# Kernel optimization log

Measured on AMD Instinct MI355X. Metric: run time of the kernel, lower is better.

Reference implementation:

```python
import jax, jax.numpy as jnp
import numpy as np

N_NODES = 100000  # static segment count for segment_sum
DEGREE = 2        # polynomial degree of the Laplacian filter


def setup_inputs() -> dict:
    key = jax.random.key(0)
    k1, k2, k3, k4 = jax.random.split(key, 4)
    N, E, C = N_NODES, 1600000, 32
    x = jax.random.normal(k1, (N, C), dtype=jnp.float32)
    weights = jax.random.normal(k2, (1 + DEGREE,), dtype=jnp.float32)
    edge_src = jax.random.randint(k3, (E,), 0, N, dtype=jnp.int32)
    edge_dst = jax.random.randint(k4, (E,), 0, N, dtype=jnp.int32)
    return {"x": x, "weights": weights, "edge_src": edge_src, "edge_dst": edge_dst}


def reference(x, weights, edge_src, edge_dst):
    """y = (w0 * I + w1 * L + ... + w_d * L^d) @ x with L = D - A,
    computed by the recurrence t_k = L @ t_{k-1} (never materializing L^k)."""
    N = N_NODES
    # node degrees: D[i] = number of edges landing on i
    deg = jax.ops.segment_sum(jnp.ones_like(edge_src, dtype=x.dtype), edge_dst,
                              num_segments=N)  # [N]

    def lap_matvec(t):
        # (L @ t)[i] = deg[i] * t[i] - sum_{(s->i) in E} t[s]
        agg = jax.ops.segment_sum(t[edge_src], edge_dst, num_segments=N)  # [N, C]
        return deg[:, None] * t - agg

    y = weights[0] * x
    t = x
    for k in range(1, 1 + DEGREE):  # fixed small loop over polynomial order
        t = lap_matvec(t)
        y = y + weights[k] * t
    return y
```

## Files before the change

kernel.cpp:

```cpp
#include <hip/hip_runtime.h>

#define C 32
#define NT 256
#define BSH 8
#define BNODE 256
#define CAPC 5632
#define SRCMASK 0x1FFFF

__device__ __forceinline__ unsigned int f2bf(float f) {
    unsigned int u = __float_as_uint(f);
    return (u + 0x7FFFu + ((u >> 16) & 1u)) >> 16;
}
__device__ __forceinline__ float bflo(unsigned int u) { return __uint_as_float(u << 16); }
__device__ __forceinline__ float bfhi(unsigned int u) { return __uint_as_float(u & 0xFFFF0000u); }

__global__ void init_cursor(int* __restrict__ cursor, int nbuck) {
    int i = blockIdx.x * blockDim.x + threadIdx.x;
    if (i < nbuck) cursor[i] = i * CAPC;
}

__global__ void cvt_kernel(const float2* __restrict__ x2, unsigned int* __restrict__ xb, int n2) {
    int i = blockIdx.x * blockDim.x + threadIdx.x;
    if (i >= n2) return;
    float2 v = x2[i];
    xb[i] = f2bf(v.x) | (f2bf(v.y) << 16);
}

__global__ __launch_bounds__(1024) void phaseA(const int* __restrict__ src,
                                               const int* __restrict__ dst,
                                               int* __restrict__ cursor,
                                               int* __restrict__ pk,
                                               int E, int nbuck, int chunk) {
    extern __shared__ int l[];
    int* lcnt = l;
    int* lcur = l + nbuck;
    int tid = threadIdx.x;
    for (int i = tid; i < nbuck; i += 1024) lcnt[i] = 0;
    __syncthreads();
    int base = blockIdx.x * chunk;
    int end  = min(base + chunk, E);
    for (int e = base + tid; e < end; e += 1024)
        atomicAdd(&lcnt[dst[e] >> BSH], 1);
    __syncthreads();
    for (int i = tid; i < nbuck; i += 1024) {
        int c = lcnt[i];
        lcur[i] = c ? atomicAdd(&cursor[i], c) : 0;
    }
    __syncthreads();
    for (int e = base + tid; e < end; e += 1024) {
        int d = dst[e];
        int b = d >> BSH;
        int pos = atomicAdd(&lcur[b], 1);
        pk[pos] = src[e] | ((d & (BNODE - 1)) << 17);
    }
}

__global__ __launch_bounds__(512) void phaseB(int* __restrict__ pk,
                                              const int* __restrict__ cursor,
                                              int* __restrict__ row_start,
                                              int* __restrict__ ideg, int N) {
    __shared__ int ent[CAPC];
    __shared__ int h[BNODE];
    __shared__ int s[BNODE];
    __shared__ int cur[BNODE];
    int b = blockIdx.x;
    int tid = threadIdx.x;
    int base = b * CAPC;
    int cnt = min(cursor[b] - base, CAPC);
    for (int i = tid; i < cnt; i += 512) ent[i] = pk[base + i];
    if (tid < BNODE) h[tid] = 0;
    __syncthreads();
    for (int i = tid; i < cnt; i += 512) atomicAdd(&h[ent[i] >> 17], 1);
    __syncthreads();
    int v = 0;
    if (tid < BNODE) { v = h[tid]; s[tid] = v; }
    __syncthreads();
    for (int off = 1; off < BNODE; off <<= 1) {
        int u = 0;
        if (tid < BNODE && tid >= off) u = s[tid - off];
        __syncthreads();
        if (tid < BNODE) s[tid] += u;
        __syncthreads();
    }
    if (tid < BNODE) {
        int exc = s[tid] - v;
        int n = (b << BSH) + tid;
        if (n < N) { row_start[n] = base + exc; ideg[n] = v; }
        cur[tid] = exc;
    }
    __syncthreads();
    for (int i = tid; i < cnt; i += 512) {
        int en = ent[i];
        int pos = atomicAdd(&cur[en >> 17], 1);
        pk[base + pos] = en & SRCMASK;
    }
}

__global__ __launch_bounds__(NT) void gather1_bf(const float* __restrict__ x,
        const unsigned int* __restrict__ xb, const int* __restrict__ pk,
        const int* __restrict__ row_start, const int* __restrict__ ideg,
        float* __restrict__ t1, unsigned int* __restrict__ t1b, int N) {
    int g = blockIdx.x * blockDim.x + threadIdx.x;
    int n = g >> 4;
    if (n >= N) return;
    int l = g & 15;
    int rs = row_start[n];
    int dg = ideg[n];
    int re = rs + dg;
    float ax0=0,ay0=0,ax1=0,ay1=0,ax2=0,ay2=0,ax3=0,ay3=0;
    int j = rs;
    for (; j + 3 < re; j += 4) {
        int s0 = pk[j], s1 = pk[j+1], s2 = pk[j+2], s3 = pk[j+3];
        unsigned int u0 = xb[s0*16 + l], u1 = xb[s1*16 + l];
        unsigned int u2 = xb[s2*16 + l], u3 = xb[s3*16 + l];
        ax0 += bflo(u0); ay0 += bfhi(u0);
        ax1 += bflo(u1); ay1 += bfhi(u1);
        ax2 += bflo(u2); ay2 += bfhi(u2);
        ax3 += bflo(u3); ay3 += bfhi(u3);
    }
    for (; j < re; ++j) { unsigned int u = xb[pk[j]*16 + l]; ax0 += bflo(u); ay0 += bfhi(u); }
    float sx = (ax0+ax1)+(ax2+ax3), sy = (ay0+ay1)+(ay2+ay3);
    size_t o = (size_t)n * C + l * 2;
    float2 xv = *(const float2*)(x + o);
    float fdg = (float)dg;
    float2 tv; tv.x = fdg * xv.x - sx; tv.y = fdg * xv.y - sy;
    *(float2*)(t1 + o) = tv;
    t1b[n*16 + l] = f2bf(tv.x) | (f2bf(tv.y) << 16);
}

__global__ __launch_bounds__(NT) void gather2_bf(const float* __restrict__ x,
        const float* __restrict__ t1, const unsigned int* __restrict__ t1b,
        const int* __restrict__ pk, const int* __restrict__ row_start,
        const int* __restrict__ ideg, const float* __restrict__ wts,
        float* __restrict__ y, int N) {
    int g = blockIdx.x * blockDim.x + threadIdx.x;
    int n = g >> 4;
    if (n >= N) return;
    int l = g & 15;
    int rs = row_start[n];
    int dg = ideg[n];
    int re = rs + dg;
    float ax0=0,ay0=0,ax1=0,ay1=0,ax2=0,ay2=0,ax3=0,ay3=0;
    int j = rs;
    for (; j + 3 < re; j += 4) {
        int s0 = pk[j], s1 = pk[j+1], s2 = pk[j+2], s3 = pk[j+3];
        unsigned int u0 = t1b[s0*16 + l], u1 = t1b[s1*16 + l];
        unsigned int u2 = t1b[s2*16 + l], u3 = t1b[s3*16 + l];
        ax0 += bflo(u0); ay0 += bfhi(u0);
        ax1 += bflo(u1); ay1 += bfhi(u1);
        ax2 += bflo(u2); ay2 += bfhi(u2);
        ax3 += bflo(u3); ay3 += bfhi(u3);
    }
    for (; j < re; ++j) { unsigned int u = t1b[pk[j]*16 + l]; ax0 += bflo(u); ay0 += bfhi(u); }
    float sx = (ax0+ax1)+(ax2+ax3), sy = (ay0+ay1)+(ay2+ay3);
    size_t o = (size_t)n * C + l * 2;
    float2 xv = *(const float2*)(x + o);
    float2 tv = *(const float2*)(t1 + o);
    float w0 = wts[0], w1 = wts[1], w2 = wts[2];
    float fdg = (float)dg;
    float2 r;
    r.x = w0 * xv.x + w1 * tv.x + w2 * (fdg * tv.x - sx);
    r.y = w0 * xv.y + w1 * tv.y + w2 * (fdg * tv.y - sy);
    *(float2*)(y + o) = r;
}

__global__ __launch_bounds__(NT) void gather1_f32(const float* __restrict__ x,
        const int* __restrict__ pk, const int* __restrict__ row_start,
        const int* __restrict__ ideg, float* __restrict__ t1, int N) {
    int g = blockIdx.x * blockDim.x + threadIdx.x;
    int n = g >> 5;
    if (n >= N) return;
    int ch = g & 31;
    int rs = row_start[n], dg = ideg[n], re = rs + dg;
    float a0=0,a1=0,a2=0,a3=0;
    int j = rs;
    for (; j + 3 < re; j += 4) {
        a0 += x[(size_t)pk[j]*C + ch];   a1 += x[(size_t)pk[j+1]*C + ch];
        a2 += x[(size_t)pk[j+2]*C + ch]; a3 += x[(size_t)pk[j+3]*C + ch];
    }
    for (; j < re; ++j) a0 += x[(size_t)pk[j]*C + ch];
    size_t o = (size_t)n*C + ch;
    t1[o] = (float)dg * x[o] - ((a0+a1)+(a2+a3));
}
__global__ __launch_bounds__(NT) void gather2_f32(const float* __restrict__ x,
        const float* __restrict__ t1, const int* __restrict__ pk,
        const int* __restrict__ row_start, const int* __restrict__ ideg,
        const float* __restrict__ wts, float* __restrict__ y, int N) {
    int g = blockIdx.x * blockDim.x + threadIdx.x;
    int n = g >> 5;
    if (n >= N) return;
    int ch = g & 31;
    int rs = row_start[n], dg = ideg[n], re = rs + dg;
    float a0=0,a1=0,a2=0,a3=0;
    int j = rs;
    for (; j + 3 < re; j += 4) {
        a0 += t1[(size_t)pk[j]*C + ch];   a1 += t1[(size_t)pk[j+1]*C + ch];
        a2 += t1[(size_t)pk[j+2]*C + ch]; a3 += t1[(size_t)pk[j+3]*C + ch];
    }
    for (; j < re; ++j) a0 += t1[(size_t)pk[j]*C + ch];
    size_t o = (size_t)n*C + ch;
    float tv = t1[o];
    y[o] = wts[0]*x[o] + wts[1]*tv + wts[2]*((float)dg*tv - ((a0+a1)+(a2+a3)));
}

extern "C" void kernel_launch(void* const* d_in, const int* in_sizes, int n_in,
                              void* d_out, int out_size, void* d_ws, size_t ws_size,
                              hipStream_t stream) {
    const float* x    = (const float*)d_in[0];
    const float* wts  = (const float*)d_in[1];
    const int*   esrc = (const int*)d_in[2];
    const int*   edst = (const int*)d_in[3];
    float*       y    = (float*)d_out;

    const int N = in_sizes[0] / C;
    const int E = in_sizes[2];
    const int nbuck = (N + BNODE - 1) >> BSH;
    const int nc = N * C;

    char* p = (char*)d_ws;
    auto align16 = [](size_t s) { return (s + 15) & ~(size_t)15; };
    int* cursor    = (int*)p; p += align16((size_t)nbuck * 4);
    int* row_start = (int*)p; p += align16((size_t)N * 4);
    int* ideg      = (int*)p; p += align16((size_t)N * 4);
    int* pk        = (int*)p; p += align16((size_t)nbuck * CAPC * 4);
    float* t1      = (float*)p; p += align16((size_t)nc * 4);
    unsigned int* xb  = (unsigned int*)p; p += align16((size_t)nc * 2);
    unsigned int* t1b = (unsigned int*)p; p += align16((size_t)nc * 2);
    bool bf_ok = (size_t)(p - (char*)d_ws) <= ws_size;

    init_cursor<<<(nbuck + NT - 1) / NT, NT, 0, stream>>>(cursor, nbuck);

    const int ABLK = 256;
    const int chunk = (E + ABLK - 1) / ABLK;
    const size_t lds_a = (size_t)nbuck * 2 * 4;
    phaseA<<<ABLK, 1024, lds_a, stream>>>(esrc, edst, cursor, pk, E, nbuck, chunk);
    phaseB<<<nbuck, 512, 0, stream>>>(pk, cursor, row_start, ideg, N);

    if (bf_ok) {
        const int n2 = nc / 2;
        cvt_kernel<<<(n2 + NT - 1) / NT, NT, 0, stream>>>((const float2*)x, xb, n2);
        const int gblocks = ((size_t)N * 16 + NT - 1) / NT;
        gather1_bf<<<gblocks, NT, 0, stream>>>(x, xb, pk, row_start, ideg, t1, t1b, N);
        gather2_bf<<<gblocks, NT, 0, stream>>>(x, t1, t1b, pk, row_start, ideg, wts, y, N);
    } else {
        const int gblocks = ((size_t)N * 32 + NT - 1) / NT;
        gather1_f32<<<gblocks, NT, 0, stream>>>(x, pk, row_start, ideg, t1, N);
        gather2_f32<<<gblocks, NT, 0, stream>>>(x, t1, pk, row_start, ideg, wts, y, N);
    }
}
```

Measured before the change: 174.9 us.

## Fuse bf16 conversion into phaseB and widen gathers to 8 lanes per node

Removes the separate conversion kernel by folding the fp32-to-bf16 conversion of x into phaseB, which already runs one block per 256-node bucket. The gather kernels now use 8 lanes per node, each loading a uint2 (4 bf16 channels), and unroll the edge loop by 8 to keep more loads in flight. Edge-index and dense x/t1/y accesses use nontemporal loads and stores to limit cache pollution. Fewer threads per node lowers parallelism, and the conversion adds work to phaseB.

Result: no change. 175.0 us (+0.1%).

```diff
diff --git a/kernel.cpp b/kernel.cpp
--- a/kernel.cpp
+++ b/kernel.cpp
@@ -7,6 +7,8 @@
 #define CAPC 5632
 #define SRCMASK 0x1FFFF
 
+typedef float f32x4 __attribute__((ext_vector_type(4)));
+
 __device__ __forceinline__ unsigned int f2bf(float f) {
     unsigned int u = __float_as_uint(f);
     return (u + 0x7FFFu + ((u >> 16) & 1u)) >> 16;
@@ -17,13 +19,6 @@
 __global__ void init_cursor(int* __restrict__ cursor, int nbuck) {
     int i = blockIdx.x * blockDim.x + threadIdx.x;
     if (i < nbuck) cursor[i] = i * CAPC;
-}
-
-__global__ void cvt_kernel(const float2* __restrict__ x2, unsigned int* __restrict__ xb, int n2) {
-    int i = blockIdx.x * blockDim.x + threadIdx.x;
-    if (i >= n2) return;
-    float2 v = x2[i];
-    xb[i] = f2bf(v.x) | (f2bf(v.y) << 16);
 }
 
 __global__ __launch_bounds__(1024) void phaseA(const int* __restrict__ src,
@@ -58,13 +53,28 @@
 __global__ __launch_bounds__(512) void phaseB(int* __restrict__ pk,
                                               const int* __restrict__ cursor,
                                               int* __restrict__ row_start,
-                                              int* __restrict__ ideg, int N) {
+                                              int* __restrict__ ideg,
+                                              const float* __restrict__ x,
+                                              uint2* __restrict__ xb2, int N) {
     __shared__ int ent[CAPC];
     __shared__ int h[BNODE];
     __shared__ int s[BNODE];
     __shared__ int cur[BNODE];
     int b = blockIdx.x;
     int tid = threadIdx.x;
+
+    int n0 = b << BSH;
+    int nvalid = min(N - n0, BNODE);
+    for (int i = tid; i < nvalid * 8; i += 512) {
+        int n = n0 + (i >> 3);
+        int lq = i & 7;
+        const float* xp = x + (size_t)n * C + lq * 4;
+        uint2 r;
+        r.x = f2bf(xp[0]) | (f2bf(xp[1]) << 16);
+        r.y = f2bf(xp[2]) | (f2bf(xp[3]) << 16);
+        xb2[(size_t)n * 8 + lq] = r;
+    }
+
     int base = b * CAPC;
     int cnt = min(cursor[b] - base, CAPC);
     for (int i = tid; i < cnt; i += 512) ent[i] = pk[base + i];
@@ -84,7 +94,7 @@
     }
     if (tid < BNODE) {
         int exc = s[tid] - v;
-        int n = (b << BSH) + tid;
+        int n = n0 + tid;
         if (n < N) { row_start[n] = base + exc; ideg[n] = v; }
         cur[tid] = exc;
     }
@@ -96,72 +106,125 @@
     }
 }
 
+#define ACC4(u0, u1)                                     \
+    a0 += bflo(u0); a1 += bfhi(u0);                      \
+    a2 += bflo(u1); a3 += bfhi(u1);
+
 __global__ __launch_bounds__(NT) void gather1_bf(const float* __restrict__ x,
-        const unsigned int* __restrict__ xb, const int* __restrict__ pk,
+        const uint2* __restrict__ xb2, const int* __restrict__ pk,
         const int* __restrict__ row_start, const int* __restrict__ ideg,
-        float* __restrict__ t1, unsigned int* __restrict__ t1b, int N) {
+        float* __restrict__ t1, uint2* __restrict__ t1b2, int N) {
     int g = blockIdx.x * blockDim.x + threadIdx.x;
-    int n = g >> 4;
+    int n = g >> 3;
     if (n >= N) return;
-    int l = g & 15;
+    int lq = g & 7;
     int rs = row_start[n];
     int dg = ideg[n];
     int re = rs + dg;
-    float ax0=0,ay0=0,ax1=0,ay1=0,ax2=0,ay2=0,ax3=0,ay3=0;
+    float a0 = 0.f, a1 = 0.f, a2 = 0.f, a3 = 0.f;
     int j = rs;
-    for (; j + 3 < re; j += 4) {
-        int s0 = pk[j], s1 = pk[j+1], s2 = pk[j+2], s3 = pk[j+3];
-        unsigned int u0 = xb[s0*16 + l], u1 = xb[s1*16 + l];
-        unsigned int u2 = xb[s2*16 + l], u3 = xb[s3*16 + l];
-        ax0 += bflo(u0); ay0 += bfhi(u0);
-        ax1 += bflo(u1); ay1 += bfhi(u1);
-        ax2 += bflo(u2); ay2 += bfhi(u2);
-        ax3 += bflo(u3); ay3 += bfhi(u3);
-    }
-    for (; j < re; ++j) { unsigned int u = xb[pk[j]*16 + l]; ax0 += bflo(u); ay0 += bfhi(u); }
-    float sx = (ax0+ax1)+(ax2+ax3), sy = (ay0+ay1)+(ay2+ay3);
-    size_t o = (size_t)n * C + l * 2;
-    float2 xv = *(const float2*)(x + o);
+    for (; j + 7 < re; j += 8) {
+        int s0 = __builtin_nontemporal_load(&pk[j]);
+        int s1 = __builtin_nontemporal_load(&pk[j + 1]);
+        int s2 = __builtin_nontemporal_load(&pk[j + 2]);
+        int s3 = __builtin_nontemporal_load(&pk[j + 3]);
+        int s4 = __builtin_nontemporal_load(&pk[j + 4]);
+        int s5 = __builtin_nontemporal_load(&pk[j + 5]);
+        int s6 = __builtin_nontemporal_load(&pk[j + 6]);
+        int s7 = __builtin_nontemporal_load(&pk[j + 7]);
+        uint2 u0 = xb2[(size_t)s0 * 8 + lq];
+        uint2 u1 = xb2[(size_t)s1 * 8 + lq];
+        uint2 u2 = xb2[(size_t)s2 * 8 + lq];
+        uint2 u3 = xb2[(size_t)s3 * 8 + lq];
+        uint2 u4 = xb2[(size_t)s4 * 8 + lq];
+        uint2 u5 = xb2[(size_t)s5 * 8 + lq];
+        uint2 u6 = xb2[(size_t)s6 * 8 + lq];
+        uint2 u7 = xb2[(size_t)s7 * 8 + lq];
+        ACC4(u0.x, u0.y) ACC4(u1.x, u1.y) ACC4(u2.x, u2.y) ACC4(u3.x, u3.y)
+        ACC4(u4.x, u4.y) ACC4(u5.x, u5.y) ACC4(u6.x, u6.y) ACC4(u7.x, u7.y)
+    }
+    for (; j + 1 < re; j += 2) {
+        int s0 = __builtin_nontemporal_load(&pk[j]);
+        int s1 = __builtin_nontemporal_load(&pk[j + 1]);
+        uint2 u0 = xb2[(size_t)s0 * 8 + lq];
+        uint2 u1 = xb2[(size_t)s1 * 8 + lq];
+        ACC4(u0.x, u0.y) ACC4(u1.x, u1.y)
+    }
+    if (j < re) {
+        uint2 u0 = xb2[(size_t)__builtin_nontemporal_load(&pk[j]) * 8 + lq];
+        ACC4(u0.x, u0.y)
+    }
+    size_t o = (size_t)n * C + lq * 4;
+    f32x4 xv = __builtin_nontemporal_load((const f32x4*)(x + o));
     float fdg = (float)dg;
-    float2 tv; tv.x = fdg * xv.x - sx; tv.y = fdg * xv.y - sy;
-    *(float2*)(t1 + o) = tv;
-    t1b[n*16 + l] = f2bf(tv.x) | (f2bf(tv.y) << 16);
+    f32x4 tv;
+    tv.x = fdg * xv.x - a0;
+    tv.y = fdg * xv.y - a1;
+    tv.z = fdg * xv.z - a2;
+    tv.w = fdg * xv.w - a3;
+    __builtin_nontemporal_store(tv, (f32x4*)(t1 + o));
+    uint2 r;
+    r.x = f2bf(tv.x) | (f2bf(tv.y) << 16);
+    r.y = f2bf(tv.z) | (f2bf(tv.w) << 16);
+    t1b2[(size_t)n * 8 + lq] = r;
 }
 
 __global__ __launch_bounds__(NT) void gather2_bf(const float* __restrict__ x,
-        const float* __restrict__ t1, const unsigned int* __restrict__ t1b,
+        const float* __restrict__ t1, const uint2* __restrict__ t1b2,
         const int* __restrict__ pk, const int* __restrict__ row_start,
         const int* __restrict__ ideg, const float* __restrict__ wts,
         float* __restrict__ y, int N) {
     int g = blockIdx.x * blockDim.x + threadIdx.x;
-    int n = g >> 4;
+    int n = g >> 3;
     if (n >= N) return;
-    int l = g & 15;
+    int lq = g & 7;
     int rs = row_start[n];
     int dg = ideg[n];
     int re = rs + dg;
-    float ax0=0,ay0=0,ax1=0,ay1=0,ax2=0,ay2=0,ax3=0,ay3=0;
+    float a0 = 0.f, a1 = 0.f, a2 = 0.f, a3 = 0.f;
     int j = rs;
-    for (; j + 3 < re; j += 4) {
-        int s0 = pk[j], s1 = pk[j+1], s2 = pk[j+2], s3 = pk[j+3];
-        unsigned int u0 = t1b[s0*16 + l], u1 = t1b[s1*16 + l];
-        unsigned int u2 = t1b[s2*16 + l], u3 = t1b[s3*16 + l];
-        ax0 += bflo(u0); ay0 += bfhi(u0);
-        ax1 += bflo(u1); ay1 += bfhi(u1);
-        ax2 += bflo(u2); ay2 += bfhi(u2);
-        ax3 += bflo(u3); ay3 += bfhi(u3);
-    }
-    for (; j < re; ++j) { unsigned int u = t1b[pk[j]*16 + l]; ax0 += bflo(u); ay0 += bfhi(u); }
-    float sx = (ax0+ax1)+(ax2+ax3), sy = (ay0+ay1)+(ay2+ay3);
-    size_t o = (size_t)n * C + l * 2;
-    float2 xv = *(const float2*)(x + o);
-    float2 tv = *(const float2*)(t1 + o);
+    for (; j + 7 < re; j += 8) {
+        int s0 = __builtin_nontemporal_load(&pk[j]);
+        int s1 = __builtin_nontemporal_load(&pk[j + 1]);
+        int s2 = __builtin_nontemporal_load(&pk[j + 2]);
+        int s3 = __builtin_nontemporal_load(&pk[j + 3]);
+        int s4 = __builtin_nontemporal_load(&pk[j + 4]);
+        int s5 = __builtin_nontemporal_load(&pk[j + 5]);
+        int s6 = __builtin_nontemporal_load(&pk[j + 6]);
+        int s7 = __builtin_nontemporal_load(&pk[j + 7]);
+        uint2 u0 = t1b2[(size_t)s0 * 8 + lq];
+        uint2 u1 = t1b2[(size_t)s1 * 8 + lq];
+        uint2 u2 = t1b2[(size_t)s2 * 8 + lq];
+        uint2 u3 = t1b2[(size_t)s3 * 8 + lq];
+        uint2 u4 = t1b2[(size_t)s4 * 8 + lq];
+        uint2 u5 = t1b2[(size_t)s5 * 8 + lq];
+        uint2 u6 = t1b2[(size_t)s6 * 8 + lq];
+        uint2 u7 = t1b2[(size_t)s7 * 8 + lq];
+        ACC4(u0.x, u0.y) ACC4(u1.x, u1.y) ACC4(u2.x, u2.y) ACC4(u3.x, u3.y)
+        ACC4(u4.x, u4.y) ACC4(u5.x, u5.y) ACC4(u6.x, u6.y) ACC4(u7.x, u7.y)
+    }
+    for (; j + 1 < re; j += 2) {
+        int s0 = __builtin_nontemporal_load(&pk[j]);
+        int s1 = __builtin_nontemporal_load(&pk[j + 1]);
+        uint2 u0 = t1b2[(size_t)s0 * 8 + lq];
+        uint2 u1 = t1b2[(size_t)s1 * 8 + lq];
+        ACC4(u0.x, u0.y) ACC4(u1.x, u1.y)
+    }
+    if (j < re) {
+        uint2 u0 = t1b2[(size_t)__builtin_nontemporal_load(&pk[j]) * 8 + lq];
+        ACC4(u0.x, u0.y)
+    }
+    size_t o = (size_t)n * C + lq * 4;
+    f32x4 xv = __builtin_nontemporal_load((const f32x4*)(x + o));
+    f32x4 tv = __builtin_nontemporal_load((const f32x4*)(t1 + o));
     float w0 = wts[0], w1 = wts[1], w2 = wts[2];
     float fdg = (float)dg;
-    float2 r;
-    r.x = w0 * xv.x + w1 * tv.x + w2 * (fdg * tv.x - sx);
-    r.y = w0 * xv.y + w1 * tv.y + w2 * (fdg * tv.y - sy);
-    *(float2*)(y + o) = r;
+    f32x4 r;
+    r.x = w0 * xv.x + w1 * tv.x + w2 * (fdg * tv.x - a0);
+    r.y = w0 * xv.y + w1 * tv.y + w2 * (fdg * tv.y - a1);
+    r.z = w0 * xv.z + w1 * tv.z + w2 * (fdg * tv.z - a2);
+    r.w = w0 * xv.w + w1 * tv.w + w2 * (fdg * tv.w - a3);
+    __builtin_nontemporal_store(r, (f32x4*)(y + o));
 }
 
 __global__ __launch_bounds__(NT) void gather1_f32(const float* __restrict__ x,
@@ -172,15 +235,15 @@
     if (n >= N) return;
     int ch = g & 31;
     int rs = row_start[n], dg = ideg[n], re = rs + dg;
-    float a0=0,a1=0,a2=0,a3=0;
+    float a0 = 0, a1 = 0, a2 = 0, a3 = 0;
     int j = rs;
     for (; j + 3 < re; j += 4) {
-        a0 += x[(size_t)pk[j]*C + ch];   a1 += x[(size_t)pk[j+1]*C + ch];
-        a2 += x[(size_t)pk[j+2]*C + ch]; a3 += x[(size_t)pk[j+3]*C + ch];
-    }
-    for (; j < re; ++j) a0 += x[(size_t)pk[j]*C + ch];
-    size_t o = (size_t)n*C + ch;
-    t1[o] = (float)dg * x[o] - ((a0+a1)+(a2+a3));
+        a0 += x[(size_t)pk[j] * C + ch];     a1 += x[(size_t)pk[j + 1] * C + ch];
+        a2 += x[(size_t)pk[j + 2] * C + ch]; a3 += x[(size_t)pk[j + 3] * C + ch];
+    }
+    for (; j < re; ++j) a0 += x[(size_t)pk[j] * C + ch];
+    size_t o = (size_t)n * C + ch;
+    t1[o] = (float)dg * x[o] - ((a0 + a1) + (a2 + a3));
 }
 __global__ __launch_bounds__(NT) void gather2_f32(const float* __restrict__ x,
         const float* __restrict__ t1, const int* __restrict__ pk,
@@ -191,16 +254,16 @@
     if (n >= N) return;
     int ch = g & 31;
     int rs = row_start[n], dg = ideg[n], re = rs + dg;
-    float a0=0,a1=0,a2=0,a3=0;
+    float a0 = 0, a1 = 0, a2 = 0, a3 = 0;
     int j = rs;
     for (; j + 3 < re; j += 4) {
-        a0 += t1[(size_t)pk[j]*C + ch];   a1 += t1[(size_t)pk[j+1]*C + ch];
-        a2 += t1[(size_t)pk[j+2]*C + ch]; a3 += t1[(size_t)pk[j+3]*C + ch];
-    }
-    for (; j < re; ++j) a0 += t1[(size_t)pk[j]*C + ch];
-    size_t o = (size_t)n*C + ch;
+        a0 += t1[(size_t)pk[j] * C + ch];     a1 += t1[(size_t)pk[j + 1] * C + ch];
+        a2 += t1[(size_t)pk[j + 2] * C + ch]; a3 += t1[(size_t)pk[j + 3] * C + ch];
+    }
+    for (; j < re; ++j) a0 += t1[(size_t)pk[j] * C + ch];
+    size_t o = (size_t)n * C + ch;
     float tv = t1[o];
-    y[o] = wts[0]*x[o] + wts[1]*tv + wts[2]*((float)dg*tv - ((a0+a1)+(a2+a3)));
+    y[o] = wts[0] * x[o] + wts[1] * tv + wts[2] * ((float)dg * tv - ((a0 + a1) + (a2 + a3)));
 }
 
 extern "C" void kernel_launch(void* const* d_in, const int* in_sizes, int n_in,
@@ -224,8 +287,8 @@
     int* ideg      = (int*)p; p += align16((size_t)N * 4);
     int* pk        = (int*)p; p += align16((size_t)nbuck * CAPC * 4);
     float* t1      = (float*)p; p += align16((size_t)nc * 4);
-    unsigned int* xb  = (unsigned int*)p; p += align16((size_t)nc * 2);
-    unsigned int* t1b = (unsigned int*)p; p += align16((size_t)nc * 2);
+    uint2* xb2     = (uint2*)p; p += align16((size_t)nc * 2);
+    uint2* t1b2    = (uint2*)p; p += align16((size_t)nc * 2);
     bool bf_ok = (size_t)(p - (char*)d_ws) <= ws_size;
 
     init_cursor<<<(nbuck + NT - 1) / NT, NT, 0, stream>>>(cursor, nbuck);
@@ -234,14 +297,12 @@
     const int chunk = (E + ABLK - 1) / ABLK;
     const size_t lds_a = (size_t)nbuck * 2 * 4;
     phaseA<<<ABLK, 1024, lds_a, stream>>>(esrc, edst, cursor, pk, E, nbuck, chunk);
-    phaseB<<<nbuck, 512, 0, stream>>>(pk, cursor, row_start, ideg, N);
+    phaseB<<<nbuck, 512, 0, stream>>>(pk, cursor, row_start, ideg, x, xb2, N);
 
     if (bf_ok) {
-        const int n2 = nc / 2;
-        cvt_kernel<<<(n2 + NT - 1) / NT, NT, 0, stream>>>((const float2*)x, xb, n2);
-        const int gblocks = ((size_t)N * 16 + NT - 1) / NT;
-        gather1_bf<<<gblocks, NT, 0, stream>>>(x, xb, pk, row_start, ideg, t1, t1b, N);
-        gather2_bf<<<gblocks, NT, 0, stream>>>(x, t1, t1b, pk, row_start, ideg, wts, y, N);
+        const int gblocks = ((size_t)N * 8 + NT - 1) / NT;
+        gather1_bf<<<gblocks, NT, 0, stream>>>(x, xb2, pk, row_start, ideg, t1, t1b2, N);
+        gather2_bf<<<gblocks, NT, 0, stream>>>(x, t1, t1b2, pk, row_start, ideg, wts, y, N);
     } else {
         const int gblocks = ((size_t)N * 32 + NT - 1) / NT;
         gather1_f32<<<gblocks, NT, 0, stream>>>(x, pk, row_start, ideg, t1, N);
```
